# Optimization experiments

Measured on AMD Instinct MI355X. Metric: run time of the kernel, lower is better.

Reference implementation:

```python
import jax, jax.numpy as jnp
import numpy as np

N, E, F_IN, H, D = 50000, 800000, 128, 4, 32


def setup_inputs() -> dict:
    key = jax.random.key(0)
    k1, k2, k3, k4 = jax.random.split(key, 4)
    feat = jax.random.normal(k1, (N, F_IN), dtype=jnp.float32)
    src = jax.random.randint(k2, (E,), 0, N, dtype=jnp.int64)
    dst = jax.random.randint(k3, (E,), 0, N, dtype=jnp.int64)
    # fc weight (xavier-normal-ish scale) and explicit bias
    W = jax.random.normal(k4, (F_IN, H * D), dtype=jnp.float32) * (1.0 / np.sqrt(F_IN))
    bias = jnp.zeros((H * D,), dtype=jnp.float32)
    return {"feat": feat, "src": src, "dst": dst, "W": W, "bias": bias}


def reference(feat, src, dst, W, bias):
    # fc projection, view as (N, H, D)
    ft = (feat @ W).reshape(N, H, D)
    # apply_edges u_dot_v: per-edge per-head dot product -> [E, H]
    e = jnp.einsum("ehd,ehd->eh", ft[src], ft[dst])
    # edge_softmax over incoming edges of each dst node (numerically stable)
    emax = jax.ops.segment_max(e, dst, num_segments=N)  # [N, H]
    ex = jnp.exp(e - emax[dst])
    denom = jax.ops.segment_sum(ex, dst, num_segments=N)  # [N, H]
    a = ex / denom[dst]  # [E, H]
    # update_all: u_mul_e + sum -> weighted scatter aggregation
    msg = ft[src] * a[:, :, None]  # [E, H, D]
    rst = jax.ops.segment_sum(msg, dst, num_segments=N)  # [N, H, D]
    return rst + bias.reshape(1, H, D)
```

## Files before the change

### kernel.cpp

```cpp
#include <hip/hip_runtime.h>
#include <math.h>

#define F 128
#define HEADS 4
#define DHEAD 32
#define HIST_H 128
#define CW_MAX 6592

typedef unsigned short ushort_t;
typedef __attribute__((ext_vector_type(8))) short short8;
typedef __attribute__((ext_vector_type(4))) float f32x4;

__device__ __forceinline__ ushort_t f2bf(float x) {
  unsigned u = __float_as_uint(x);
  unsigned r = u + 0x7FFFu + ((u >> 16) & 1u);
  return (ushort_t)(r >> 16);
}

__device__ __forceinline__ void unpack8(const int4& r, float* v) {
  int rr[4] = {r.x, r.y, r.z, r.w};
#pragma unroll
  for (int q = 0; q < 4; q++) {
    unsigned u = (unsigned)rr[q];
    v[2 * q] = __uint_as_float(u << 16);
    v[2 * q + 1] = __uint_as_float(u & 0xFFFF0000u);
  }
}

__global__ __launch_bounds__(256) void wprep_kernel(
    const float* __restrict__ W, ushort_t* __restrict__ whi,
    ushort_t* __restrict__ wlo) {
  int idx = blockIdx.x * 256 + threadIdx.x;
  if (idx >= 128 * 128) return;
  int j = idx & 7;
  int lane = (idx >> 3) & 63;
  int f = idx >> 9;
  int kt = f >> 3, nt = f & 7;
  int k = kt * 32 + (lane >> 4) * 8 + j;
  int n = nt * 16 + (lane & 15);
  float w = W[k * 128 + n];
  unsigned u = __float_as_uint(w);
  unsigned hb = u & 0xFFFF0000u;
  float lo = w - __uint_as_float(hb);
  whi[idx] = (ushort_t)(hb >> 16);
  wlo[idx] = f2bf(lo);
}

__global__ __launch_bounds__(256) void gemm_hist_kernel(
    const float* __restrict__ feat, const ushort_t* __restrict__ whi,
    const ushort_t* __restrict__ wlo, ushort_t* __restrict__ ftb, int N,
    const int* __restrict__ dst, ushort_t* __restrict__ partials, int cwp,
    int E, int gemmBlocks) {
  __shared__ int lh[CW_MAX];
  if ((int)blockIdx.x >= gemmBlocks) {
    const int hb = blockIdx.x - gemmBlocks;
    const int cls = hb & 7;
    const int h = hb >> 3;
    const int cw = (N + 7) >> 3;
    const int nbase = cls * cw;
    for (int j = threadIdx.x; j < cw; j += 256) lh[j] = 0;
    __syncthreads();
    const int seg = (E + HIST_H - 1) / HIST_H;
    const int e0 = h * seg;
    const int e1 = min(e0 + seg, E);
    int e = e0 + (int)threadIdx.x;
    for (; e + 768 < e1; e += 1024) {
      int d0 = dst[e];
      int d1 = dst[e + 256];
      int d2 = dst[e + 512];
      int d3 = dst[e + 768];
      if ((unsigned)(d0 - nbase) < (unsigned)cw) atomicAdd(&lh[d0 - nbase], 1);
      if ((unsigned)(d1 - nbase) < (unsigned)cw) atomicAdd(&lh[d1 - nbase], 1);
      if ((unsigned)(d2 - nbase) < (unsigned)cw) atomicAdd(&lh[d2 - nbase], 1);
      if ((unsigned)(d3 - nbase) < (unsigned)cw) atomicAdd(&lh[d3 - nbase], 1);
    }
    for (; e < e1; e += 256) {
      int d = dst[e];
      if ((unsigned)(d - nbase) < (unsigned)cw) atomicAdd(&lh[d - nbase], 1);
    }
    __syncthreads();
    ushort_t* prow = partials + (size_t)(cls * HIST_H + h) * cwp;
    for (int j = threadIdx.x; j < cw; j += 256) prow[j] = (ushort_t)lh[j];
    return;
  }
  const int t = threadIdx.x;
  const int wv = t >> 6;
  const int l = t & 63;
  const int g = l >> 4;
  const int lm = l & 15;
  const int arow = blockIdx.x * 64 + wv * 16 + lm;
  const int arowc = min(arow, N - 1);

  f32x4 acc[8];
#pragma unroll
  for (int nt = 0; nt < 8; nt++) acc[nt] = (f32x4){0.f, 0.f, 0.f, 0.f};

#pragma unroll
  for (int kt = 0; kt < 4; kt++) {
    const float* ap = feat + (size_t)arowc * F + kt * 32 + g * 8;
    float a[8];
    *(float4*)&a[0] = *(const float4*)ap;
    *(float4*)&a[4] = *(const float4*)(ap + 4);
    short8 ahi, alo;
#pragma unroll
    for (int j = 0; j < 8; j++) {
      unsigned u = __float_as_uint(a[j]);
      unsigned hb2 = u & 0xFFFF0000u;
      float lo = a[j] - __uint_as_float(hb2);
      ahi[j] = (short)(hb2 >> 16);
      alo[j] = (short)f2bf(lo);
    }
    const ushort_t* bh = whi + (size_t)(kt * 8) * 512 + l * 8;
    const ushort_t* bl = wlo + (size_t)(kt * 8) * 512 + l * 8;
#pragma unroll
    for (int nt = 0; nt < 8; nt++) {
      short8 bhi = *(const short8*)(bh + nt * 512);
      short8 blo = *(const short8*)(bl + nt * 512);
      acc[nt] =
          __builtin_amdgcn_mfma_f32_16x16x32_bf16(ahi, blo, acc[nt], 0, 0, 0);
      acc[nt] =
          __builtin_amdgcn_mfma_f32_16x16x32_bf16(alo, bhi, acc[nt], 0, 0, 0);
      acc[nt] =
          __builtin_amdgcn_mfma_f32_16x16x32_bf16(ahi, bhi, acc[nt], 0, 0, 0);
    }
  }

  const int orow0 = blockIdx.x * 64 + wv * 16 + g * 4;
#pragma unroll
  for (int reg = 0; reg < 4; reg++) {
    int orow = orow0 + reg;
    if (orow < N) {
#pragma unroll
      for (int nt = 0; nt < 8; nt++)
        ftb[(size_t)orow * F + nt * 16 + lm] = f2bf(acc[nt][reg]);
    }
  }
}

__global__ void scan_block_kernel(const ushort_t* __restrict__ partials,
                                  int cwp, int* __restrict__ counts,
                                  int* __restrict__ offs,
                                  int* __restrict__ bsums, int N) {
  __shared__ int s[256];
  int t = threadIdx.x, i = blockIdx.x * 256 + t;
  int v = 0;
  if (i < N) {
    int cw = (N + 7) >> 3;
    int c = i / cw;
    int j = i - c * cw;
    const ushort_t* base = partials + (size_t)c * HIST_H * cwp + j;
#pragma unroll 8
    for (int h = 0; h < HIST_H; h++) v += base[(size_t)h * cwp];
    counts[i] = v;
  }
  s[t] = v;
  __syncthreads();
  for (int d = 1; d < 256; d <<= 1) {
    int x = (t >= d) ? s[t - d] : 0;
    __syncthreads();
    s[t] += x;
    __syncthreads();
  }
  if (i < N) offs[i] = s[t] - v;
  if (t == 255) bsums[blockIdx.x] = s[255];
}

__global__ void scan_finish_kernel(int* __restrict__ offs,
                                   const int* __restrict__ bsums,
                                   const ushort_t* __restrict__ partials,
                                   ushort_t* __restrict__ rel16, int cwp,
                                   int N) {
  int t = threadIdx.x, b = blockIdx.x;
  int v = (t < b) ? bsums[t] : 0;
#pragma unroll
  for (int d = 32; d > 0; d >>= 1) v += __shfl_down(v, d, 64);
  __shared__ int wsum[4];
  if ((t & 63) == 0) wsum[t >> 6] = v;
  __syncthreads();
  int total = wsum[0] + wsum[1] + wsum[2] + wsum[3];
  int i = b * 256 + t;
  if (i < N) {
    offs[i] += total;
    int cw = (N + 7) >> 3;
    int c = i / cw;
    int j = i - c * cw;
    const ushort_t* pb = partials + (size_t)c * HIST_H * cwp + j;
    ushort_t* cb = rel16 + (size_t)c * HIST_H * cwp + j;
    int run = 0;
#pragma unroll 8
    for (int h = 0; h < HIST_H; h++) {
      cb[(size_t)h * cwp] = (ushort_t)run;
      run += pb[(size_t)h * cwp];
    }
  }
}

__global__ __launch_bounds__(256) void scatter_kernel(
    const int* __restrict__ src, const int* __restrict__ dst,
    const int* __restrict__ offs, const ushort_t* __restrict__ rel16, int cwp,
    int* __restrict__ csr, int E, int N) {
  __shared__ int lcur[CW_MAX];
  const int cls = blockIdx.x & 7;
  const int h = blockIdx.x >> 3;
  const int cw = (N + 7) >> 3;
  const int nbase = cls * cw;
  const int jmax = min(cw, N - nbase);
  const ushort_t* crow = rel16 + (size_t)(cls * HIST_H + h) * cwp;
  for (int j = threadIdx.x; j < jmax; j += 256)
    lcur[j] = offs[nbase + j] + (int)crow[j];
  __syncthreads();
  const int seg = (E + HIST_H - 1) / HIST_H;
  const int e0 = h * seg;
  const int e1 = min(e0 + seg, E);
  int e = e0 + (int)threadIdx.x;
  for (; e + 768 < e1; e += 1024) {
    int d0 = dst[e];
    int d1 = dst[e + 256];
    int d2 = dst[e + 512];
    int d3 = dst[e + 768];
    int s0 = src[e];
    int s1 = src[e + 256];
    int s2 = src[e + 512];
    int s3 = src[e + 768];
    if ((unsigned)(d0 - nbase) < (unsigned)cw)
      csr[atomicAdd(&lcur[d0 - nbase], 1)] = s0;
    if ((unsigned)(d1 - nbase) < (unsigned)cw)
      csr[atomicAdd(&lcur[d1 - nbase], 1)] = s1;
    if ((unsigned)(d2 - nbase) < (unsigned)cw)
      csr[atomicAdd(&lcur[d2 - nbase], 1)] = s2;
    if ((unsigned)(d3 - nbase) < (unsigned)cw)
      csr[atomicAdd(&lcur[d3 - nbase], 1)] = s3;
  }
  for (; e < e1; e += 256) {
    int d = dst[e];
    int sv = src[e];
    if ((unsigned)(d - nbase) < (unsigned)cw)
      csr[atomicAdd(&lcur[d - nbase], 1)] = sv;
  }
}

__global__ __launch_bounds__(256) void aggregate_kernel(
    const ushort_t* __restrict__ ftb, const int* __restrict__ offs,
    const int* __restrict__ counts, const int* __restrict__ csr,
    const float* __restrict__ bias, float* __restrict__ out, int N) {
  const int T = blockIdx.x * 256 + threadIdx.x;
  if (T >= N * 16) return;
  const int sub = T & 3;
  const int p = T >> 2;
  const int h = p & 3;
  const int n = p >> 2;
  const int dimBase = h * DHEAD + sub * 8;

  const int deg = counts[n];
  const int off = offs[n];

  float ftd[8];
  {
    int4 r = *(const int4*)&ftb[n * F + dimBase];
    unpack8(r, ftd);
  }

  const float LOG2E = 1.4426950408889634f;
  float m = -INFINITY, s = 0.f;
  float acc[8];
#pragma unroll
  for (int j = 0; j < 8; j++) acc[j] = 0.f;

#define PROCESS(RX)                                              \
  do {                                                           \
    float v[8];                                                  \
    unpack8(RX, v);                                              \
    float part = 0.f;                                            \
    _Pragma("unroll") for (int j = 0; j < 8; j++) part =         \
        fmaf(ftd[j], v[j], part);                                \
    part += __shfl_xor(part, 1, 4);                              \
    part += __shfl_xor(part, 2, 4);                              \
    float el = part * LOG2E;                                     \
    float mn = fmaxf(m, el);                                     \
    float scale = exp2f(m - mn);                                 \
    float w = exp2f(el - mn);                                    \
    s = fmaf(s, scale, w);                                       \
    _Pragma("unroll") for (int j = 0; j < 8; j++) acc[j] =       \
        fmaf(acc[j], scale, w * v[j]);                           \
    m = mn;                                                      \
  } while (0)

  int4 R0 = make_int4(0, 0, 0, 0), R1 = R0, R2 = R0, R3 = R0;
  if (deg > 0) {
    int dm1 = deg - 1;
    int s0 = csr[off];
    int s1 = csr[off + min(1, dm1)];
    int s2 = csr[off + min(2, dm1)];
    int s3 = csr[off + min(3, dm1)];
    R0 = *(const int4*)&ftb[s0 * F + dimBase];
    R1 = *(const int4*)&ftb[s1 * F + dimBase];
    R2 = *(const int4*)&ftb[s2 * F + dimBase];
    R3 = *(const int4*)&ftb[s3 * F + dimBase];
  }
  int i = 0;
  for (; i + 4 <= deg; i += 4) {
    int dm1 = deg - 1;
    int sa = csr[off + min(i + 4, dm1)];
    int sb = csr[off + min(i + 5, dm1)];
    int sc = csr[off + min(i + 6, dm1)];
    int sd = csr[off + min(i + 7, dm1)];
    int4 Na = *(const int4*)&ftb[sa * F + dimBase];
    int4 Nb = *(const int4*)&ftb[sb * F + dimBase];
    int4 Nc = *(const int4*)&ftb[sc * F + dimBase];
    int4 Nd = *(const int4*)&ftb[sd * F + dimBase];
    PROCESS(R0);
    PROCESS(R1);
    PROCESS(R2);
    PROCESS(R3);
    R0 = Na; R1 = Nb; R2 = Nc; R3 = Nd;
  }
  int r = deg - i;
  if (r > 0) PROCESS(R0);
  if (r > 1) PROCESS(R1);
  if (r > 2) PROCESS(R2);
#undef PROCESS

  float inv = (deg > 0) ? 1.f / s : 0.f;
  float4 b0 = *(const float4*)&bias[dimBase];
  float4 b1 = *(const float4*)&bias[dimBase + 4];
  float4 o0 = make_float4(acc[0] * inv + b0.x, acc[1] * inv + b0.y,
                          acc[2] * inv + b0.z, acc[3] * inv + b0.w);
  float4 o1 = make_float4(acc[4] * inv + b1.x, acc[5] * inv + b1.y,
                          acc[6] * inv + b1.z, acc[7] * inv + b1.w);
  *(float4*)&out[n * F + dimBase] = o0;
  *(float4*)&out[n * F + dimBase + 4] = o1;
}

extern "C" void kernel_launch(void* const* d_in, const int* in_sizes, int n_in,
                              void* d_out, int out_size, void* d_ws,
                              size_t ws_size, hipStream_t stream) {
  const float* feat = (const float*)d_in[0];
  const int* src = (const int*)d_in[1];
  const int* dst = (const int*)d_in[2];
  const float* W = (const float*)d_in[3];
  const float* bias = (const float*)d_in[4];
  float* out = (float*)d_out;

  const int N = in_sizes[0] / F;
  const int E = in_sizes[1];
  const int cw = (N + 7) >> 3;
  const int cwp = (cw + 31) & ~31;

  char* ws = (char*)d_ws;
  ushort_t* ftb = (ushort_t*)ws;
  size_t ftB = (size_t)N * F * sizeof(ushort_t);
  ftB = (ftB + 255) & ~(size_t)255;
  int* counts = (int*)(ws + ftB);
  int* offs = counts + N;
  int* bsums = offs + N;
  int* csr = bsums + 256;
  ushort_t* whi = (ushort_t*)(csr + E);
  ushort_t* wlo = whi + 128 * 128;
  ushort_t* partials = wlo + 128 * 128;
  ushort_t* rel16 = partials + 8 * HIST_H * cwp;

  wprep_kernel<<<64, 256, 0, stream>>>(W, whi, wlo);

  int gemmBlocks = (N + 63) / 64;
  gemm_hist_kernel<<<gemmBlocks + 8 * HIST_H, 256, 0, stream>>>(
      feat, whi, wlo, ftb, N, dst, partials, cwp, E, gemmBlocks);

  int nb = (N + 255) / 256;
  scan_block_kernel<<<nb, 256, 0, stream>>>(partials, cwp, counts, offs,
                                            bsums, N);
  scan_finish_kernel<<<nb, 256, 0, stream>>>(offs, bsums, partials, rel16,
                                             cwp, N);

  scatter_kernel<<<8 * HIST_H, 256, 0, stream>>>(src, dst, offs, rel16, cwp,
                                                 csr, E, N);

  aggregate_kernel<<<(N * 16 + 255) / 256, 256, 0, stream>>>(
      ftb, offs, counts, csr, bias, out, N);
}
```

Before: 94.45 us.

## Fuse two-pass scan into single-pass decoupled lookback; deepen aggregate prefetch

Merges the block scan and scan-finish kernels into one kernel. It uses a decoupled lookback over per-block 64-bit status words, which wprep_kernel zeroes, and drops one launch plus a second pass over the histogram partials. The counts array is removed and degree is derived from offs[n+1]-offs[n]. The aggregate loop now prefetches 8 neighbor rows instead of 4, and outputs use nontemporal stores. Lookback relies on earlier blocks being scheduled first, and the deeper prefetch raises register pressure.

Measured after the change: 102.2 us. 8.2% more time.

```diff
diff --git a/kernel.cpp b/kernel.cpp
--- a/kernel.cpp
+++ b/kernel.cpp
@@ -8,6 +8,7 @@
 #define CW_MAX 6592
 
 typedef unsigned short ushort_t;
+typedef unsigned long long u64_t;
 typedef __attribute__((ext_vector_type(8))) short short8;
 typedef __attribute__((ext_vector_type(4))) float f32x4;
 
@@ -29,7 +30,8 @@
 
 __global__ __launch_bounds__(256) void wprep_kernel(
     const float* __restrict__ W, ushort_t* __restrict__ whi,
-    ushort_t* __restrict__ wlo) {
+    ushort_t* __restrict__ wlo, u64_t* __restrict__ bstate) {
+  if (blockIdx.x == 0) bstate[threadIdx.x] = 0ULL;
   int idx = blockIdx.x * 256 + threadIdx.x;
   if (idx >= 128 * 128) return;
   int j = idx & 7;
@@ -137,21 +139,22 @@
   }
 }
 
-__global__ void scan_block_kernel(const ushort_t* __restrict__ partials,
-                                  int cwp, int* __restrict__ counts,
-                                  int* __restrict__ offs,
-                                  int* __restrict__ bsums, int N) {
+__global__ __launch_bounds__(256) void scan_kernel(
+    const ushort_t* __restrict__ partials, int cwp, int* __restrict__ offs,
+    ushort_t* __restrict__ rel16, u64_t* __restrict__ bstate, int N) {
   __shared__ int s[256];
-  int t = threadIdx.x, i = blockIdx.x * 256 + t;
+  __shared__ int sprefix;
+  const int t = threadIdx.x, b = blockIdx.x;
+  const int i = b * 256 + t;
+  const int cw = (N + 7) >> 3;
   int v = 0;
+  int c = 0, j = 0;
   if (i < N) {
-    int cw = (N + 7) >> 3;
-    int c = i / cw;
-    int j = i - c * cw;
+    c = i / cw;
+    j = i - c * cw;
     const ushort_t* base = partials + (size_t)c * HIST_H * cwp + j;
 #pragma unroll 8
     for (int h = 0; h < HIST_H; h++) v += base[(size_t)h * cwp];
-    counts[i] = v;
   }
   s[t] = v;
   __syncthreads();
@@ -161,36 +164,34 @@
     s[t] += x;
     __syncthreads();
   }
-  if (i < N) offs[i] = s[t] - v;
-  if (t == 255) bsums[blockIdx.x] = s[255];
-}
-
-__global__ void scan_finish_kernel(int* __restrict__ offs,
-                                   const int* __restrict__ bsums,
-                                   const ushort_t* __restrict__ partials,
-                                   ushort_t* __restrict__ rel16, int cwp,
-                                   int N) {
-  int t = threadIdx.x, b = blockIdx.x;
-  int v = (t < b) ? bsums[t] : 0;
-#pragma unroll
-  for (int d = 32; d > 0; d >>= 1) v += __shfl_down(v, d, 64);
-  __shared__ int wsum[4];
-  if ((t & 63) == 0) wsum[t >> 6] = v;
+  const int incl = s[t];
+  const int bsum = s[255];
+  if (t == 0) {
+    atomicExch(&bstate[b], (1ULL << 32) | (unsigned)bsum);
+    int pfx = 0;
+    for (int pb = b - 1; pb >= 0; pb--) {
+      u64_t st;
+      do {
+        st = atomicAdd(&bstate[pb], 0ULL);
+      } while ((st >> 32) == 0);
+      pfx += (int)(unsigned)st;
+      if ((st >> 32) == 2ULL) break;
+    }
+    atomicExch(&bstate[b], (2ULL << 32) | (unsigned)(pfx + bsum));
+    sprefix = pfx;
+  }
   __syncthreads();
-  int total = wsum[0] + wsum[1] + wsum[2] + wsum[3];
-  int i = b * 256 + t;
   if (i < N) {
-    offs[i] += total;
-    int cw = (N + 7) >> 3;
-    int c = i / cw;
-    int j = i - c * cw;
-    const ushort_t* pb = partials + (size_t)c * HIST_H * cwp + j;
+    const int o = sprefix + incl - v;
+    offs[i] = o;
+    if (i == N - 1) offs[N] = o + v;
+    const ushort_t* pb2 = partials + (size_t)c * HIST_H * cwp + j;
     ushort_t* cb = rel16 + (size_t)c * HIST_H * cwp + j;
     int run = 0;
 #pragma unroll 8
     for (int h = 0; h < HIST_H; h++) {
       cb[(size_t)h * cwp] = (ushort_t)run;
-      run += pb[(size_t)h * cwp];
+      run += pb2[(size_t)h * cwp];
     }
   }
 }
@@ -241,8 +242,8 @@
 
 __global__ __launch_bounds__(256) void aggregate_kernel(
     const ushort_t* __restrict__ ftb, const int* __restrict__ offs,
-    const int* __restrict__ counts, const int* __restrict__ csr,
-    const float* __restrict__ bias, float* __restrict__ out, int N) {
+    const int* __restrict__ csr, const float* __restrict__ bias,
+    float* __restrict__ out, int N) {
   const int T = blockIdx.x * 256 + threadIdx.x;
   if (T >= N * 16) return;
   const int sub = T & 3;
@@ -251,8 +252,8 @@
   const int n = p >> 2;
   const int dimBase = h * DHEAD + sub * 8;
 
-  const int deg = counts[n];
   const int off = offs[n];
+  const int deg = offs[n + 1] - off;
 
   float ftd[8];
   {
@@ -286,49 +287,75 @@
   } while (0)
 
   int4 R0 = make_int4(0, 0, 0, 0), R1 = R0, R2 = R0, R3 = R0;
+  int4 R4 = R0, R5 = R0, R6 = R0, R7 = R0;
   if (deg > 0) {
     int dm1 = deg - 1;
     int s0 = csr[off];
     int s1 = csr[off + min(1, dm1)];
     int s2 = csr[off + min(2, dm1)];
     int s3 = csr[off + min(3, dm1)];
+    int s4 = csr[off + min(4, dm1)];
+    int s5 = csr[off + min(5, dm1)];
+    int s6 = csr[off + min(6, dm1)];
+    int s7 = csr[off + min(7, dm1)];
     R0 = *(const int4*)&ftb[s0 * F + dimBase];
     R1 = *(const int4*)&ftb[s1 * F + dimBase];
     R2 = *(const int4*)&ftb[s2 * F + dimBase];
     R3 = *(const int4*)&ftb[s3 * F + dimBase];
+    R4 = *(const int4*)&ftb[s4 * F + dimBase];
+    R5 = *(const int4*)&ftb[s5 * F + dimBase];
+    R6 = *(const int4*)&ftb[s6 * F + dimBase];
+    R7 = *(const int4*)&ftb[s7 * F + dimBase];
   }
   int i = 0;
-  for (; i + 4 <= deg; i += 4) {
+  for (; i + 8 <= deg; i += 8) {
     int dm1 = deg - 1;
-    int sa = csr[off + min(i + 4, dm1)];
-    int sb = csr[off + min(i + 5, dm1)];
-    int sc = csr[off + min(i + 6, dm1)];
-    int sd = csr[off + min(i + 7, dm1)];
+    int sa = csr[off + min(i + 8, dm1)];
+    int sb = csr[off + min(i + 9, dm1)];
+    int sc = csr[off + min(i + 10, dm1)];
+    int sd = csr[off + min(i + 11, dm1)];
+    int se = csr[off + min(i + 12, dm1)];
+    int sf = csr[off + min(i + 13, dm1)];
+    int sg = csr[off + min(i + 14, dm1)];
+    int sh = csr[off + min(i + 15, dm1)];
     int4 Na = *(const int4*)&ftb[sa * F + dimBase];
     int4 Nb = *(const int4*)&ftb[sb * F + dimBase];
     int4 Nc = *(const int4*)&ftb[sc * F + dimBase];
     int4 Nd = *(const int4*)&ftb[sd * F + dimBase];
+    int4 Ne = *(const int4*)&ftb[se * F + dimBase];
+    int4 Nf = *(const int4*)&ftb[sf * F + dimBase];
+    int4 Ng = *(const int4*)&ftb[sg * F + dimBase];
+    int4 Nh = *(const int4*)&ftb[sh * F + dimBase];
     PROCESS(R0);
     PROCESS(R1);
     PROCESS(R2);
     PROCESS(R3);
+    PROCESS(R4);
+    PROCESS(R5);
+    PROCESS(R6);
+    PROCESS(R7);
     R0 = Na; R1 = Nb; R2 = Nc; R3 = Nd;
+    R4 = Ne; R5 = Nf; R6 = Ng; R7 = Nh;
   }
   int r = deg - i;
   if (r > 0) PROCESS(R0);
   if (r > 1) PROCESS(R1);
   if (r > 2) PROCESS(R2);
+  if (r > 3) PROCESS(R3);
+  if (r > 4) PROCESS(R4);
+  if (r > 5) PROCESS(R5);
+  if (r > 6) PROCESS(R6);
 #undef PROCESS
 
   float inv = (deg > 0) ? 1.f / s : 0.f;
   float4 b0 = *(const float4*)&bias[dimBase];
   float4 b1 = *(const float4*)&bias[dimBase + 4];
-  float4 o0 = make_float4(acc[0] * inv + b0.x, acc[1] * inv + b0.y,
-                          acc[2] * inv + b0.z, acc[3] * inv + b0.w);
-  float4 o1 = make_float4(acc[4] * inv + b1.x, acc[5] * inv + b1.y,
-                          acc[6] * inv + b1.z, acc[7] * inv + b1.w);
-  *(float4*)&out[n * F + dimBase] = o0;
-  *(float4*)&out[n * F + dimBase + 4] = o1;
+  f32x4 o0 = {acc[0] * inv + b0.x, acc[1] * inv + b0.y, acc[2] * inv + b0.z,
+              acc[3] * inv + b0.w};
+  f32x4 o1 = {acc[4] * inv + b1.x, acc[5] * inv + b1.y, acc[6] * inv + b1.z,
+              acc[7] * inv + b1.w};
+  __builtin_nontemporal_store(o0, (f32x4*)&out[n * F + dimBase]);
+  __builtin_nontemporal_store(o1, (f32x4*)&out[n * F + dimBase + 4]);
 }
 
 extern "C" void kernel_launch(void* const* d_in, const int* in_sizes, int n_in,
@@ -350,30 +377,27 @@
   ushort_t* ftb = (ushort_t*)ws;
   size_t ftB = (size_t)N * F * sizeof(ushort_t);
   ftB = (ftB + 255) & ~(size_t)255;
-  int* counts = (int*)(ws + ftB);
-  int* offs = counts + N;
-  int* bsums = offs + N;
-  int* csr = bsums + 256;
+  int* offs = (int*)(ws + ftB);
+  int* csr = offs + N + 1;
   ushort_t* whi = (ushort_t*)(csr + E);
   ushort_t* wlo = whi + 128 * 128;
   ushort_t* partials = wlo + 128 * 128;
   ushort_t* rel16 = partials + 8 * HIST_H * cwp;
-
-  wprep_kernel<<<64, 256, 0, stream>>>(W, whi, wlo);
+  size_t relEnd = (size_t)(rel16 + 8 * HIST_H * cwp - (ushort_t*)ws);
+  u64_t* bstate = (u64_t*)(ws + ((relEnd * 2 + 7) & ~(size_t)7));
+
+  wprep_kernel<<<64, 256, 0, stream>>>(W, whi, wlo, bstate);
 
   int gemmBlocks = (N + 63) / 64;
   gemm_hist_kernel<<<gemmBlocks + 8 * HIST_H, 256, 0, stream>>>(
       feat, whi, wlo, ftb, N, dst, partials, cwp, E, gemmBlocks);
 
   int nb = (N + 255) / 256;
-  scan_block_kernel<<<nb, 256, 0, stream>>>(partials, cwp, counts, offs,
-                                            bsums, N);
-  scan_finish_kernel<<<nb, 256, 0, stream>>>(offs, bsums, partials, rel16,
-                                             cwp, N);
+  scan_kernel<<<nb, 256, 0, stream>>>(partials, cwp, offs, rel16, bstate, N);
 
   scatter_kernel<<<8 * HIST_H, 256, 0, stream>>>(src, dst, offs, rel16, cwp,
                                                  csr, E, N);
 
-  aggregate_kernel<<<(N * 16 + 255) / 256, 256, 0, stream>>>(
-      ftb, offs, counts, csr, bias, out, N);
-}
+  aggregate_kernel<<<(N * 16 + 255) / 256, 256, 0, stream>>>(ftb, offs, csr,
+                                                             bias, out, N);
+}
```
